# Kernel optimization log

Measured on AMD Instinct MI355X. Metric: run time of the kernel, lower is better.

Reference implementation:

```python
import jax, jax.numpy as jnp
import numpy as np

B, S, D = 4, 2048, 1024
H = 16
HD = D // H  # 64
BASE = 10000.0


def _rope_cache(seq_len, dim):
    inv_freq = 1.0 / (BASE ** (jnp.arange(0, dim, 2, dtype=jnp.float32) / dim))
    t = jnp.arange(seq_len, dtype=jnp.float32)
    freqs = jnp.einsum('i,j->ij', t, inv_freq)          # [S, dim/2]
    emb = jnp.concatenate([freqs, freqs], axis=-1)      # [S, dim]
    return jnp.cos(emb), jnp.sin(emb)


def _rotate_half(x):
    x1, x2 = jnp.split(x, 2, axis=-1)
    return jnp.concatenate([-x2, x1], axis=-1)


def setup_inputs() -> dict:
    key = jax.random.key(0)
    ks = jax.random.split(key, 5)
    scale = 1.0 / np.sqrt(D)
    return {
        'x': jax.random.normal(ks[0], (B, S, D), dtype=jnp.float32),
        'Wq': jax.random.normal(ks[1], (D, D), dtype=jnp.float32) * scale,
        'Wk': jax.random.normal(ks[2], (D, D), dtype=jnp.float32) * scale,
        'Wv': jax.random.normal(ks[3], (D, D), dtype=jnp.float32) * scale,
        'Wo': jax.random.normal(ks[4], (D, D), dtype=jnp.float32) * scale,
    }


def reference(x, Wq, Wk, Wv, Wo):
    b, s, d = x.shape
    # projections (torch Linear, no bias): y = x @ W.T
    q = (x @ Wq.T).reshape(b, s, H, HD).transpose(0, 2, 1, 3)  # [B,H,S,HD]
    k = (x @ Wk.T).reshape(b, s, H, HD).transpose(0, 2, 1, 3)
    v = (x @ Wv.T).reshape(b, s, H, HD).transpose(0, 2, 1, 3)
    cos, sin = _rope_cache(s, HD)  # [S, HD]
    cos = cos[None, None]
    sin = sin[None, None]
    q = q * cos + _rotate_half(q) * sin
    k = k * cos + _rotate_half(k) * sin
    scale = 1.0 / np.sqrt(HD)
    attn = jnp.einsum('bhqd,bhkd->bhqk', q, k) * scale  # [B,H,S,S]
    attn = jax.nn.softmax(attn, axis=-1)
    out = jnp.einsum('bhqk,bhkd->bhqd', attn, v)
    out = out.transpose(0, 2, 1, 3).reshape(b, s, d)
    return out @ Wo.T
```

## Files before the change

### kernel.cpp

```cpp
#include <hip/hip_runtime.h>
#include <math.h>
#include <stdint.h>

#define BB 4
#define SS 2048
#define DDIM 1024
#define HH 16
#define HD 64
#define QKVLD 3072
#define QSCALE (0.125f * 1.44269504089f)

typedef __bf16 bf16x8 __attribute__((ext_vector_type(8)));
typedef float f32x4 __attribute__((ext_vector_type(4)));
typedef float f32x16 __attribute__((ext_vector_type(16)));
typedef int i32x4 __attribute__((ext_vector_type(4)));

__device__ __forceinline__ unsigned short f2bf(float f) {
    union { float f; unsigned u; } v; v.f = f;
    unsigned r = (v.u + 0x7FFFu + ((v.u >> 16) & 1u)) >> 16;
    return (unsigned short)r;
}
__device__ __forceinline__ void gload_lds16(const unsigned short* g, unsigned char* s) {
    __builtin_amdgcn_global_load_lds(
        (const __attribute__((address_space(1))) unsigned int*)(g),
        (__attribute__((address_space(3))) unsigned int*)(s), 16, 0, 0);
}

__global__ void prep_all(const float* __restrict__ x,
                         const float* __restrict__ Wq, const float* __restrict__ Wk,
                         const float* __restrict__ Wv, const float* __restrict__ Wo,
                         unsigned short* __restrict__ xb,
                         unsigned short* __restrict__ wqkv, unsigned short* __restrict__ wob,
                         float* __restrict__ cosT, float* __restrict__ sinT) {
    int bid = blockIdx.x;
    if (bid < 8192) {
        int i = bid * 256 + threadIdx.x;
        float4 v = ((const float4*)x)[i];
        ushort4 o;
        o.x = f2bf(v.x); o.y = f2bf(v.y); o.z = f2bf(v.z); o.w = f2bf(v.w);
        ((ushort4*)xb)[i] = o;
    } else if (bid < 12288) {
        int i = (bid - 8192) * 256 + threadIdx.x;
        int mat = i >> 18;
        int off = i & 262143;
        const float* src = (mat == 0) ? Wq : (mat == 1) ? Wk : (mat == 2) ? Wv : Wo;
        unsigned short* dst = (mat < 3) ? (wqkv + (size_t)mat * 1048576) : wob;
        float4 v = ((const float4*)src)[off];
        ushort4 o;
        o.x = f2bf(v.x); o.y = f2bf(v.y); o.z = f2bf(v.z); o.w = f2bf(v.w);
        ((ushort4*)dst)[off] = o;
    } else {
        int idx = (bid - 12288) * 256 + threadIdx.x;
        int s = idx >> 5;
        int j = idx & 31;
        float invf = powf(10000.0f, -(float)j / 32.0f);
        float ang = (float)s * invf;
        cosT[idx] = cosf(ang);
        sinT[idx] = sinf(ang);
    }
}

template <int EPI>
__global__ __launch_bounds__(256) void gemm_bf16_nt(const unsigned short* __restrict__ A,
                                                    const unsigned short* __restrict__ Bm,
                                                    void* __restrict__ C,
                                                    int M, int N, int K, int lda,
                                                    const float* __restrict__ cosT,
                                                    const float* __restrict__ sinT,
                                                    unsigned short* __restrict__ vt) {
    __shared__ unsigned char smem[32768];
    const int t = threadIdx.x;
    const int l = t & 63;
    const int w = t >> 6;
    const int wm = w >> 1, wn = w & 1;

    const int bid = blockIdx.y * gridDim.x + blockIdx.x;
    const int cpx = (gridDim.x * gridDim.y) >> 3;
    const int swz = (bid & 7) * cpx + (bid >> 3);
    const int row0 = (swz / gridDim.x) * 128;
    const int col0 = (swz % gridDim.x) * 128;

    f32x4 zero4 = {0.f, 0.f, 0.f, 0.f};
    f32x4 acc[4][4];
#pragma unroll
    for (int i = 0; i < 4; ++i)
#pragma unroll
        for (int j = 0; j < 4; ++j) acc[i][j] = zero4;

    const int srow = w * 32 + (l >> 2);
    const int scol8 = ((l & 3) ^ ((l >> 3) & 3)) << 3;
    const unsigned short* aS = A + (size_t)(row0 + srow) * lda + scol8;
    const unsigned short* bS = Bm + (size_t)(col0 + srow) * K + scol8;

    int aoff[4], boff[4];
#pragma unroll
    for (int mi = 0; mi < 4; ++mi) {
        int o = (wm * 64 + mi * 16 + (l & 15)) * 64 + ((l >> 4) << 4);
        o ^= ((o >> 7) & 3) << 4;
        aoff[mi] = o;
    }
#pragma unroll
    for (int ni = 0; ni < 4; ++ni) {
        int o = (wn * 64 + ni * 16 + (l & 15)) * 64 + ((l >> 4) << 4);
        o ^= ((o >> 7) & 3) << 4;
        boff[ni] = 8192 + o;
    }

    gload_lds16(aS,                    smem + w * 2048);
    gload_lds16(aS + (size_t)16 * lda, smem + w * 2048 + 1024);
    gload_lds16(bS,                    smem + 8192 + w * 2048);
    gload_lds16(bS + (size_t)16 * K,   smem + 8192 + w * 2048 + 1024);

    int cur = 0;
    for (int k0 = 0; k0 < K; k0 += 32) {
        const int nxt = cur ^ 1;
        if (k0 + 32 < K) {
            const unsigned short* aN = aS + k0 + 32;
            const unsigned short* bN = bS + k0 + 32;
            unsigned char* d = smem + nxt * 16384;
            gload_lds16(aN,                    d + w * 2048);
            gload_lds16(aN + (size_t)16 * lda, d + w * 2048 + 1024);
            gload_lds16(bN,                    d + 8192 + w * 2048);
            gload_lds16(bN + (size_t)16 * K,   d + 8192 + w * 2048 + 1024);
            asm volatile("s_waitcnt vmcnt(4)" ::: "memory");
        } else {
            asm volatile("s_waitcnt vmcnt(0)" ::: "memory");
        }
        __builtin_amdgcn_s_barrier();
        asm volatile("" ::: "memory");

        const unsigned char* base = smem + cur * 16384;
        bf16x8 af[4], bf[4];
#pragma unroll
        for (int mi = 0; mi < 4; ++mi) af[mi] = *(const bf16x8*)(base + aoff[mi]);
#pragma unroll
        for (int ni = 0; ni < 4; ++ni) bf[ni] = *(const bf16x8*)(base + boff[ni]);
#pragma unroll
        for (int mi = 0; mi < 4; ++mi)
#pragma unroll
            for (int ni = 0; ni < 4; ++ni)
                acc[mi][ni] = __builtin_amdgcn_mfma_f32_16x16x32_bf16(af[mi], bf[ni], acc[mi][ni], 0, 0, 0);

        asm volatile("s_waitcnt lgkmcnt(0)" ::: "memory");
        __builtin_amdgcn_s_barrier();
        asm volatile("" ::: "memory");
        cur = nxt;
    }

    const int cr = (l >> 4) << 2;
    const int cc = l & 15;

    if (EPI == 0) {
#pragma unroll
        for (int mi = 0; mi < 4; ++mi)
#pragma unroll
            for (int ni = 0; ni < 4; ++ni) {
                int gcol = col0 + wn * 64 + ni * 16 + cc;
#pragma unroll
                for (int r = 0; r < 4; ++r) {
                    int grow = row0 + wm * 64 + mi * 16 + cr + r;
                    ((float*)C)[(size_t)grow * N + gcol] = acc[mi][ni][r];
                }
            }
    } else {
        const int sec = (col0 + wn * 64) >> 10;
        if (sec == 2) {
#pragma unroll
            for (int mi = 0; mi < 4; ++mi) {
                int s0 = row0 + wm * 64 + mi * 16 + cr;
                int bI = s0 >> 11;
                int sI = s0 & (SS - 1);
#pragma unroll
                for (int ni = 0; ni < 4; ++ni) {
                    int vcol = col0 + wn * 64 + ni * 16 + cc - 2048;
                    int hh = vcol >> 6, dd = vcol & 63;
                    ushort4 o;
                    o.x = f2bf(acc[mi][ni][0]);
                    o.y = f2bf(acc[mi][ni][1]);
                    o.z = f2bf(acc[mi][ni][2]);
                    o.w = f2bf(acc[mi][ni][3]);
                    *(ushort4*)&vt[((size_t)((bI * HH + hh) * HD + dd)) * SS + sI] = o;
                }
            }
        } else {
            const float qs = (sec == 0) ? QSCALE : 1.0f;
#pragma unroll
            for (int mi = 0; mi < 4; ++mi) {
#pragma unroll
                for (int r = 0; r < 4; ++r) {
                    int grow = row0 + wm * 64 + mi * 16 + cr + r;
                    int s = grow & (SS - 1);
#pragma unroll
                    for (int ni = 0; ni < 2; ++ni) {
                        int j = ni * 16 + cc;
                        float c = cosT[(s << 5) + j];
                        float sn = sinT[(s << 5) + j];
                        float x1 = acc[mi][ni][r], x2 = acc[mi][ni + 2][r];
                        int gcol = col0 + wn * 64 + j;
                        ((unsigned short*)C)[(size_t)grow * N + gcol]      = f2bf((x1 * c - x2 * sn) * qs);
                        ((unsigned short*)C)[(size_t)grow * N + gcol + 32] = f2bf((x2 * c + x1 * sn) * qs);
                    }
                }
            }
        }
    }
}

__global__ __launch_bounds__(256) void attn_mfma10(const unsigned short* __restrict__ qkv,
                                                   const unsigned short* __restrict__ vt,
                                                   unsigned short* __restrict__ og) {
    __shared__ unsigned char smem[32768];
    const int tid = threadIdx.x;
    const int ln = tid & 63;
    const int w = tid >> 6;
    const int lq = ln & 31;
    const int hi = ln >> 5;

    const int did = blockIdx.x + (blockIdx.y << 4) + (blockIdx.z << 8);
    const int b = did & 3;
    const int h = (did >> 2) & 15;
    const int qb0 = (did >> 6) << 7;

    const int headoff = h * HD;
    const size_t bS = (size_t)b * SS;

    bf16x8 qf[4];
    {
        const unsigned short* qsrc = qkv + (bS + qb0 + w * 32 + lq) * QKVLD + headoff + hi * 8;
#pragma unroll
        for (int dc = 0; dc < 4; ++dc)
            qf[dc] = *(const bf16x8*)(qsrc + dc * 16);
    }

    f32x16 oacc[2];
#pragma unroll
    for (int i = 0; i < 2; ++i)
#pragma unroll
        for (int r = 0; r < 16; ++r) oacc[i][r] = 0.f;
    float lsum = 0.f;

    f32x16 fzero;
#pragma unroll
    for (int r = 0; r < 16; ++r) fzero[r] = 0.f;

    const int srow = w * 16 + (ln >> 3);
    const int scol = ((ln & 7) ^ (ln >> 3)) << 3;
    const unsigned short* kbase_g = qkv + bS * QKVLD + 1024 + headoff;
    const unsigned short* vtbase_g = vt + (size_t)(b * HH + h) * HD * SS;

    {
        const unsigned short* ksrc = kbase_g + (size_t)srow * QKVLD + scol;
        gload_lds16(ksrc,                     smem + w * 2048);
        gload_lds16(ksrc + (size_t)8 * QKVLD, smem + w * 2048 + 1024);
        const unsigned short* vsrc = vtbase_g + (size_t)srow * SS + scol;
        gload_lds16(vsrc,                  smem + 16384 + w * 2048);
        gload_lds16(vsrc + (size_t)8 * SS, smem + 16384 + w * 2048 + 1024);
    }
    __syncthreads();

#pragma unroll 2
    for (int tkv = 0; tkv < SS / 64; ++tkv) {
        const int cur = tkv & 1;
        const int kcur = cur * 8192;
        const int vcur = 16384 + cur * 8192;
        const int nxt = cur ^ 1;
        const bool pre = (tkv + 1 < SS / 64);
        if (pre) {
            const int kv1 = (tkv + 1) * 64;
            const unsigned short* ksrc = kbase_g + (size_t)(kv1 + srow) * QKVLD + scol;
            gload_lds16(ksrc,                     smem + nxt * 8192 + w * 2048);
            gload_lds16(ksrc + (size_t)8 * QKVLD, smem + nxt * 8192 + w * 2048 + 1024);
            const unsigned short* vsrc = vtbase_g + (size_t)srow * SS + kv1 + scol;
            gload_lds16(vsrc,                  smem + 16384 + nxt * 8192 + w * 2048);
            gload_lds16(vsrc + (size_t)8 * SS, smem + 16384 + nxt * 8192 + w * 2048 + 1024);
        }

        f32x16 st[2];
#pragma unroll
        for (int kb = 0; kb < 2; ++kb) {
            bf16x8 kf[4];
#pragma unroll
            for (int dc = 0; dc < 4; ++dc) {
                int row = kb * 32 + lq;
                int o = kcur + ((row * 128 + dc * 32 + hi * 16) ^ ((row & 7) << 4));
                kf[dc] = *(const bf16x8*)(smem + o);
            }
            __builtin_amdgcn_s_setprio(1);
            st[kb] = __builtin_amdgcn_mfma_f32_32x32x16_bf16(kf[0], qf[0], fzero, 0, 0, 0);
#pragma unroll
            for (int dc = 1; dc < 4; ++dc)
                st[kb] = __builtin_amdgcn_mfma_f32_32x32x16_bf16(kf[dc], qf[dc], st[kb], 0, 0, 0);
            __builtin_amdgcn_s_setprio(0);
        }

        float pg[32];
#pragma unroll
        for (int j = 0; j < 16; ++j) pg[j] = __builtin_amdgcn_exp2f(st[0][j]);
#pragma unroll
        for (int j = 0; j < 16; ++j) pg[16 + j] = __builtin_amdgcn_exp2f(st[1][j]);

        i32x4 pwv[4];
#pragma unroll
        for (int g = 0; g < 4; ++g) {
            unsigned u0, u1, u2, u3;
            asm("v_cvt_pk_bf16_f32 %0, %1, %2" : "=v"(u0) : "v"(pg[g * 8 + 0]), "v"(pg[g * 8 + 1]));
            asm("v_cvt_pk_bf16_f32 %0, %1, %2" : "=v"(u1) : "v"(pg[g * 8 + 2]), "v"(pg[g * 8 + 3]));
            asm("v_cvt_pk_bf16_f32 %0, %1, %2" : "=v"(u2) : "v"(pg[g * 8 + 4]), "v"(pg[g * 8 + 5]));
            asm("v_cvt_pk_bf16_f32 %0, %1, %2" : "=v"(u3) : "v"(pg[g * 8 + 6]), "v"(pg[g * 8 + 7]));
            asm("v_permlane32_swap_b32 %0, %1" : "+v"(u0), "+v"(u2));
            asm("v_permlane32_swap_b32 %0, %1" : "+v"(u1), "+v"(u3));
            pwv[g][0] = (int)u0; pwv[g][1] = (int)u1; pwv[g][2] = (int)u2; pwv[g][3] = (int)u3;
        }

        float rs;
        {
            float s0 = (pg[0] + pg[1]) + (pg[2] + pg[3]);
            float s1 = (pg[4] + pg[5]) + (pg[6] + pg[7]);
            float s2 = (pg[8] + pg[9]) + (pg[10] + pg[11]);
            float s3 = (pg[12] + pg[13]) + (pg[14] + pg[15]);
            float s4 = (pg[16] + pg[17]) + (pg[18] + pg[19]);
            float s5 = (pg[20] + pg[21]) + (pg[22] + pg[23]);
            float s6 = (pg[24] + pg[25]) + (pg[26] + pg[27]);
            float s7 = (pg[28] + pg[29]) + (pg[30] + pg[31]);
            rs = ((s0 + s1) + (s2 + s3)) + ((s4 + s5) + (s6 + s7));
        }
        rs += __shfl_xor(rs, 32);
        lsum += rs;

        __builtin_amdgcn_s_setprio(1);
#pragma unroll
        for (int dblk = 0; dblk < 2; ++dblk) {
#pragma unroll
            for (int ks = 0; ks < 4; ++ks) {
                int row = dblk * 32 + lq;
                int o = vcur + ((row * 128 + ks * 32 + hi * 16) ^ ((row & 7) << 4));
                bf16x8 vf = *(const bf16x8*)(smem + o);
                oacc[dblk] = __builtin_amdgcn_mfma_f32_32x32x16_bf16(
                    __builtin_bit_cast(bf16x8, pwv[ks]), vf, oacc[dblk], 0, 0, 0);
            }
        }
        __builtin_amdgcn_s_setprio(0);

        __syncthreads();
    }

    {
        float inv = 1.0f / lsum;
#pragma unroll
        for (int r = 0; r < 16; ++r) {
            int crow = (r & 3) + 8 * (r >> 2) + 4 * hi;
            float invr = __shfl(inv, crow);
            int grow = qb0 + w * 32 + crow;
            size_t base = (bS + grow) * QKVLD + headoff + lq;
            og[base]      = f2bf(oacc[0][r] * invr);
            og[base + 32] = f2bf(oacc[1][r] * invr);
        }
    }
}

extern "C" void kernel_launch(void* const* d_in, const int* in_sizes, int n_in,
                              void* d_out, int out_size, void* d_ws, size_t ws_size,
                              hipStream_t stream) {
    const float* x  = (const float*)d_in[0];
    const float* Wq = (const float*)d_in[1];
    const float* Wk = (const float*)d_in[2];
    const float* Wv = (const float*)d_in[3];
    const float* Wo = (const float*)d_in[4];
    float* out = (float*)d_out;

    const size_t BSD = (size_t)BB * SS * DDIM;
    const size_t WSZ = (size_t)DDIM * DDIM;

    unsigned short* xb   = (unsigned short*)d_ws;
    unsigned short* wqkv = xb + BSD;
    unsigned short* wob  = wqkv + 3 * WSZ;
    unsigned short* qkv  = wob + WSZ;
    unsigned short* vt   = qkv + (size_t)BB * SS * QKVLD;
    float* cosT = (float*)(vt + BSD);
    float* sinT = cosT + (size_t)SS * 32;

    dim3 blk(256);

    hipLaunchKernelGGL(prep_all, dim3(12544), blk, 0, stream,
                       x, Wq, Wk, Wv, Wo, xb, wqkv, wob, cosT, sinT);

    hipLaunchKernelGGL((gemm_bf16_nt<2>), dim3(QKVLD / 128, BB * SS / 128), blk, 0, stream,
                       xb, wqkv, (void*)qkv, BB * SS, QKVLD, DDIM, DDIM, cosT, sinT, vt);

    hipLaunchKernelGGL(attn_mfma10, dim3(SS / 128, HH, BB), blk, 0, stream, qkv, vt, qkv);

    hipLaunchKernelGGL((gemm_bf16_nt<0>), dim3(DDIM / 128, BB * SS / 128), blk, 0, stream,
                       qkv, wob, (void*)out, BB * SS, DDIM, DDIM, QKVLD, nullptr, nullptr, nullptr);
}
```

Measured before the change: 198.6 us.

## Use 256x256 tiled 512-thread pipelined GEMM for fused QKV projection

Replaces the templated 128x128 GEMM used for the QKV projection with a dedicated kernel that uses 256x256 tiles, 8 waves, and 128KB of LDS. The new kernel double-buffers A and B, staggers their prefetch, splits each k-tile into four phases that interleave loads with MFMAs, and raises wave priority around the MFMA blocks. The aim is more operand reuse per byte loaded and better overlap of global-to-LDS traffic with compute. In exchange the grid is only 12x32 blocks and the kernel needs large LDS and many registers, which lowers occupancy and may leave CUs unevenly loaded. The output projection keeps the old kernel with only its fp32 epilogue.

```diff
diff --git a/kernel.cpp b/kernel.cpp
--- a/kernel.cpp
+++ b/kernel.cpp
@@ -60,14 +60,162 @@
     }
 }
 
-template <int EPI>
-__global__ __launch_bounds__(256) void gemm_bf16_nt(const unsigned short* __restrict__ A,
-                                                    const unsigned short* __restrict__ Bm,
-                                                    void* __restrict__ C,
-                                                    int M, int N, int K, int lda,
-                                                    const float* __restrict__ cosT,
-                                                    const float* __restrict__ sinT,
-                                                    unsigned short* __restrict__ vt) {
+__global__ __launch_bounds__(512) void gemm256_qkv(const unsigned short* __restrict__ A,
+                                                   const unsigned short* __restrict__ Bm,
+                                                   unsigned short* __restrict__ C,
+                                                   const float* __restrict__ cosT,
+                                                   const float* __restrict__ sinT,
+                                                   unsigned short* __restrict__ vt) {
+    __shared__ unsigned char smem[131072];
+    const int t = threadIdx.x;
+    const int l = t & 63;
+    const int w = t >> 6;
+    const int wm = w >> 2;
+    const int wn = w & 3;
+    const int K = DDIM;
+    const int NT = K >> 6;
+
+    const int bid = blockIdx.y * gridDim.x + blockIdx.x;
+    const int cpx = (gridDim.x * gridDim.y) >> 3;
+    const int swz = (bid & 7) * cpx + (bid >> 3);
+    const int row0 = (swz / gridDim.x) * 256;
+    const int col0 = (swz % gridDim.x) * 256;
+
+    f32x4 acc[8][4];
+#pragma unroll
+    for (int i = 0; i < 8; ++i)
+#pragma unroll
+        for (int j = 0; j < 4; ++j) acc[i][j] = f32x4{0.f, 0.f, 0.f, 0.f};
+
+    const unsigned short* aSg = A + (size_t)(row0 + w * 16 + (l >> 3)) * K + ((l & 7) ^ (l >> 3)) * 8;
+    const unsigned short* bSg = Bm + (size_t)(col0 + w * 16 + (l >> 3)) * K + ((l & 7) ^ (l >> 3)) * 8;
+    const int dRow = (w * 16) * 128;
+
+#define STAGE_A(kt, h, j, buf) \
+    gload_lds16(aSg + (size_t)((h) * 128 + (j) * 8) * K + (kt) * 64, \
+                smem + (buf) * 65536 + (h) * 16384 + dRow + (j) * 1024)
+#define STAGE_B(kt, h, j, buf) \
+    gload_lds16(bSg + (size_t)((h) * 128 + (j) * 8) * K + (kt) * 64, \
+                smem + (buf) * 65536 + 32768 + (h) * 16384 + dRow + (j) * 1024)
+
+    STAGE_B(0, 0, 0, 0); STAGE_B(0, 0, 1, 0); STAGE_B(0, 1, 0, 0); STAGE_B(0, 1, 1, 0);
+    STAGE_A(0, 0, 0, 0); STAGE_A(0, 0, 1, 0); STAGE_A(0, 1, 0, 0); STAGE_A(0, 1, 1, 0);
+    STAGE_B(1, 0, 0, 1); STAGE_B(1, 0, 1, 1); STAGE_B(1, 1, 0, 1); STAGE_B(1, 1, 1, 1);
+    asm volatile("s_waitcnt vmcnt(4)" ::: "memory");
+    __builtin_amdgcn_s_barrier();
+
+    const int cA = (l >> 4) << 4;
+    const int swr = (l & 7) << 4;
+    const int rA0 = wm * 128 + (l & 15);
+    const int rB0 = wn * 64 + (l & 15);
+
+    int cur = 0;
+    for (int u = 0; u < NT; ++u) {
+        const int nxt = cur ^ 1;
+        const unsigned char* Ab = smem + cur * 65536;
+        const unsigned char* Bb = smem + cur * 65536 + 32768;
+        const bool pA = (u + 1 < NT);
+        const bool pB = (u + 2 < NT);
+        bf16x8 bfr[4][2];
+
+#pragma unroll
+        for (int p = 0; p < 4; ++p) {
+            if (p == 0) { if (pA) { STAGE_A(u + 1, 0, 0, nxt); STAGE_A(u + 1, 0, 1, nxt); } }
+            if (p == 1) { if (pA) { STAGE_A(u + 1, 1, 0, nxt); STAGE_A(u + 1, 1, 1, nxt); } }
+            if (p == 2) { if (pB) { STAGE_B(u + 2, 0, 0, cur); STAGE_B(u + 2, 0, 1, cur); } }
+            if (p == 3) { if (pB) { STAGE_B(u + 2, 1, 0, cur); STAGE_B(u + 2, 1, 1, cur); } }
+
+            if (p == 0) {
+#pragma unroll
+                for (int ni = 0; ni < 4; ++ni)
+#pragma unroll
+                    for (int kk = 0; kk < 2; ++kk) {
+                        int row = rB0 + ni * 16;
+                        bfr[ni][kk] = *(const bf16x8*)(Bb + (row * 128 + ((kk * 64 + cA) ^ swr)));
+                    }
+            }
+            bf16x8 af[2][2];
+#pragma unroll
+            for (int m2 = 0; m2 < 2; ++m2)
+#pragma unroll
+                for (int kk = 0; kk < 2; ++kk) {
+                    int row = rA0 + (p * 2 + m2) * 16;
+                    af[m2][kk] = *(const bf16x8*)(Ab + (row * 128 + ((kk * 64 + cA) ^ swr)));
+                }
+
+            __builtin_amdgcn_s_barrier();
+            asm volatile("s_waitcnt lgkmcnt(0)" ::: "memory");
+            __builtin_amdgcn_sched_barrier(0);
+            __builtin_amdgcn_s_setprio(1);
+#pragma unroll
+            for (int m2 = 0; m2 < 2; ++m2)
+#pragma unroll
+                for (int ni = 0; ni < 4; ++ni)
+#pragma unroll
+                    for (int kk = 0; kk < 2; ++kk)
+                        acc[p * 2 + m2][ni] = __builtin_amdgcn_mfma_f32_16x16x32_bf16(
+                            af[m2][kk], bfr[ni][kk], acc[p * 2 + m2][ni], 0, 0, 0);
+            __builtin_amdgcn_s_setprio(0);
+            if (p == 3) {
+                if (u < NT - 2) asm volatile("s_waitcnt vmcnt(4)" ::: "memory");
+                else            asm volatile("s_waitcnt vmcnt(0)" ::: "memory");
+            }
+            __builtin_amdgcn_s_barrier();
+        }
+        cur = nxt;
+    }
+#undef STAGE_A
+#undef STAGE_B
+
+    const int cr = (l >> 4) << 2;
+    const int cc = l & 15;
+    const int sec = (col0 + wn * 64) >> 10;
+
+    if (sec == 2) {
+#pragma unroll
+        for (int mi = 0; mi < 8; ++mi) {
+            int s0 = row0 + wm * 128 + mi * 16 + cr;
+            int bI = s0 >> 11;
+            int sI = s0 & (SS - 1);
+#pragma unroll
+            for (int ni = 0; ni < 4; ++ni) {
+                int vcol = col0 + wn * 64 + ni * 16 + cc - 2048;
+                int hh = vcol >> 6, dd = vcol & 63;
+                ushort4 o;
+                o.x = f2bf(acc[mi][ni][0]);
+                o.y = f2bf(acc[mi][ni][1]);
+                o.z = f2bf(acc[mi][ni][2]);
+                o.w = f2bf(acc[mi][ni][3]);
+                *(ushort4*)&vt[((size_t)((bI * HH + hh) * HD + dd)) * SS + sI] = o;
+            }
+        }
+    } else {
+        const float qs = (sec == 0) ? QSCALE : 1.0f;
+#pragma unroll
+        for (int mi = 0; mi < 8; ++mi) {
+#pragma unroll
+            for (int r = 0; r < 4; ++r) {
+                int grow = row0 + wm * 128 + mi * 16 + cr + r;
+                int s = grow & (SS - 1);
+#pragma unroll
+                for (int ni = 0; ni < 2; ++ni) {
+                    int j = ni * 16 + cc;
+                    float c = cosT[(s << 5) + j];
+                    float sn = sinT[(s << 5) + j];
+                    float x1 = acc[mi][ni][r], x2 = acc[mi][ni + 2][r];
+                    int gcol = col0 + wn * 64 + j;
+                    C[(size_t)grow * QKVLD + gcol]      = f2bf((x1 * c - x2 * sn) * qs);
+                    C[(size_t)grow * QKVLD + gcol + 32] = f2bf((x2 * c + x1 * sn) * qs);
+                }
+            }
+        }
+    }
+}
+
+__global__ __launch_bounds__(256) void gemm_bf16_out(const unsigned short* __restrict__ A,
+                                                     const unsigned short* __restrict__ Bm,
+                                                     float* __restrict__ C,
+                                                     int M, int N, int K, int lda) {
     __shared__ unsigned char smem[32768];
     const int t = threadIdx.x;
     const int l = t & 63;
@@ -80,12 +228,11 @@
     const int row0 = (swz / gridDim.x) * 128;
     const int col0 = (swz % gridDim.x) * 128;
 
-    f32x4 zero4 = {0.f, 0.f, 0.f, 0.f};
     f32x4 acc[4][4];
 #pragma unroll
     for (int i = 0; i < 4; ++i)
 #pragma unroll
-        for (int j = 0; j < 4; ++j) acc[i][j] = zero4;
+        for (int j = 0; j < 4; ++j) acc[i][j] = f32x4{0.f, 0.f, 0.f, 0.f};
 
     const int srow = w * 32 + (l >> 2);
     const int scol8 = ((l & 3) ^ ((l >> 3) & 3)) << 3;
@@ -149,61 +296,17 @@
 
     const int cr = (l >> 4) << 2;
     const int cc = l & 15;
-
-    if (EPI == 0) {
-#pragma unroll
-        for (int mi = 0; mi < 4; ++mi)
-#pragma unroll
-            for (int ni = 0; ni < 4; ++ni) {
-                int gcol = col0 + wn * 64 + ni * 16 + cc;
-#pragma unroll
-                for (int r = 0; r < 4; ++r) {
-                    int grow = row0 + wm * 64 + mi * 16 + cr + r;
-                    ((float*)C)[(size_t)grow * N + gcol] = acc[mi][ni][r];
-                }
-            }
-    } else {
-        const int sec = (col0 + wn * 64) >> 10;
-        if (sec == 2) {
-#pragma unroll
-            for (int mi = 0; mi < 4; ++mi) {
-                int s0 = row0 + wm * 64 + mi * 16 + cr;
-                int bI = s0 >> 11;
-                int sI = s0 & (SS - 1);
-#pragma unroll
-                for (int ni = 0; ni < 4; ++ni) {
-                    int vcol = col0 + wn * 64 + ni * 16 + cc - 2048;
-                    int hh = vcol >> 6, dd = vcol & 63;
-                    ushort4 o;
-                    o.x = f2bf(acc[mi][ni][0]);
-                    o.y = f2bf(acc[mi][ni][1]);
-                    o.z = f2bf(acc[mi][ni][2]);
-                    o.w = f2bf(acc[mi][ni][3]);
-                    *(ushort4*)&vt[((size_t)((bI * HH + hh) * HD + dd)) * SS + sI] = o;
-                }
-            }
-        } else {
-            const float qs = (sec == 0) ? QSCALE : 1.0f;
-#pragma unroll
-            for (int mi = 0; mi < 4; ++mi) {
-#pragma unroll
-                for (int r = 0; r < 4; ++r) {
-                    int grow = row0 + wm * 64 + mi * 16 + cr + r;
-                    int s = grow & (SS - 1);
-#pragma unroll
-                    for (int ni = 0; ni < 2; ++ni) {
-                        int j = ni * 16 + cc;
-                        float c = cosT[(s << 5) + j];
-                        float sn = sinT[(s << 5) + j];
-                        float x1 = acc[mi][ni][r], x2 = acc[mi][ni + 2][r];
-                        int gcol = col0 + wn * 64 + j;
-                        ((unsigned short*)C)[(size_t)grow * N + gcol]      = f2bf((x1 * c - x2 * sn) * qs);
-                        ((unsigned short*)C)[(size_t)grow * N + gcol + 32] = f2bf((x2 * c + x1 * sn) * qs);
-                    }
-                }
-            }
-        }
-    }
+#pragma unroll
+    for (int mi = 0; mi < 4; ++mi)
+#pragma unroll
+        for (int ni = 0; ni < 4; ++ni) {
+            int gcol = col0 + wn * 64 + ni * 16 + cc;
+#pragma unroll
+            for (int r = 0; r < 4; ++r) {
+                int grow = row0 + wm * 64 + mi * 16 + cr + r;
+                C[(size_t)grow * N + gcol] = acc[mi][ni][r];
+            }
+        }
 }
 
 __global__ __launch_bounds__(256) void attn_mfma10(const unsigned short* __restrict__ qkv,
@@ -379,16 +482,14 @@
     float* cosT = (float*)(vt + BSD);
     float* sinT = cosT + (size_t)SS * 32;
 
-    dim3 blk(256);
-
-    hipLaunchKernelGGL(prep_all, dim3(12544), blk, 0, stream,
+    hipLaunchKernelGGL(prep_all, dim3(12544), dim3(256), 0, stream,
                        x, Wq, Wk, Wv, Wo, xb, wqkv, wob, cosT, sinT);
 
-    hipLaunchKernelGGL((gemm_bf16_nt<2>), dim3(QKVLD / 128, BB * SS / 128), blk, 0, stream,
-                       xb, wqkv, (void*)qkv, BB * SS, QKVLD, DDIM, DDIM, cosT, sinT, vt);
-
-    hipLaunchKernelGGL(attn_mfma10, dim3(SS / 128, HH, BB), blk, 0, stream, qkv, vt, qkv);
-
-    hipLaunchKernelGGL((gemm_bf16_nt<0>), dim3(DDIM / 128, BB * SS / 128), blk, 0, stream,
-                       qkv, wob, (void*)out, BB * SS, DDIM, DDIM, QKVLD, nullptr, nullptr, nullptr);
-}
+    hipLaunchKernelGGL(gemm256_qkv, dim3(QKVLD / 256, BB * SS / 256), dim3(512), 0, stream,
+                       xb, wqkv, qkv, cosT, sinT, vt);
+
+    hipLaunchKernelGGL(attn_mfma10, dim3(SS / 128, HH, BB), dim3(256), 0, stream, qkv, vt, qkv);
+
+    hipLaunchKernelGGL(gemm_bf16_out, dim3(DDIM / 128, BB * SS / 128), dim3(256), 0, stream,
+                       qkv, wob, out, BB * SS, DDIM, DDIM, QKVLD);
+}
```

New measurement: 193.7 us. 2.5% less time.
